# Optimization experiments

Hardware: AMD Instinct MI355X
Metric: run time of the kernel (lower is better)

The kernel has to match this reference:

```python
import jax, jax.numpy as jnp
import numpy as np

N = 1024
HID, STEM_CH = 256, 64
BN_OUT, ST_OUT, MLP = 128, 64, 256
MORPH, BN_WS, ST_WS = 31, 11, 31
FH = FW = 256
VH = VW = 1024
VIS_PS, FUSED_PS = 0.1, 0.4
DELTA_SCALE, EPS = 1.5, 1e-8


def _gauss(ws):
    y = np.linspace(-1.0, 1.0, ws)
    yy, xx = np.meshgrid(y, y, indexing='ij')
    g = np.exp(-(xx ** 2 + yy ** 2) / (2 * 0.4 ** 2))
    return jnp.asarray((g / g.sum())[None, None], dtype=jnp.float32)

BN_GAUSS = _gauss(BN_WS)
ST_GAUSS = _gauss(ST_WS)


def _gelu(x):
    return jax.nn.gelu(x, approximate=False)


def _softplus_inverse(x, eps=1e-6):
    x = jnp.maximum(x, eps)
    return x + jnp.log(-jnp.expm1(-x))


def _normalise(t, eps=EPS):
    t = jnp.maximum(t, 0.0)
    return t / (t.sum(axis=(-2, -1), keepdims=True) + eps)


def _extract_windows(fmap, pos, ws):
    # fmap: [1,C,H,W]; pos: [N,2] = (x,y) float pixel coords -> [N,C,ws,ws] via bilinear gather
    f = fmap[0]
    C, H, W = f.shape
    half = ws // 2
    offs = jnp.arange(ws, dtype=pos.dtype) - half
    xs = jnp.clip(pos[:, 0:1] + offs, 0.0, W - 1.0)  # [N,ws]
    ys = jnp.clip(pos[:, 1:2] + offs, 0.0, H - 1.0)
    x0 = jnp.clip(jnp.floor(xs), 0, W - 2).astype(jnp.int32)
    y0 = jnp.clip(jnp.floor(ys), 0, H - 2).astype(jnp.int32)
    wx = (xs - x0)[:, None, :]   # [N,1,ws]
    wy = (ys - y0)[:, :, None]   # [N,ws,1]
    X0, Y0 = x0[:, None, :], y0[:, :, None]
    v00 = f[:, Y0, X0]
    v01 = f[:, Y0, X0 + 1]
    v10 = f[:, Y0 + 1, X0]
    v11 = f[:, Y0 + 1, X0 + 1]   # each [C,N,ws,ws]
    out = (v00 * (1 - wy) * (1 - wx) + v01 * (1 - wy) * wx
           + v10 * wy * (1 - wx) + v11 * wy * wx)
    return out.transpose(1, 0, 2, 3)


def _convnext_block(x, dw_w, dw_b, ln_g, ln_b, pw1_w, pw1_b, pw2_w, pw2_b, gamma):
    C = x.shape[1]
    h = jax.lax.conv_general_dilated(x, dw_w, (1, 1), [(3, 3), (3, 3)],
        dimension_numbers=('NCHW', 'OIHW', 'NCHW'), feature_group_count=C)
    h = h + dw_b[None, :, None, None]
    h = h.transpose(0, 2, 3, 1)  # NHWC
    mu = h.mean(-1, keepdims=True)
    var = ((h - mu) ** 2).mean(-1, keepdims=True)
    h = (h - mu) / jnp.sqrt(var + 1e-6) * ln_g + ln_b
    h = _gelu(h @ pw1_w.T + pw1_b)
    h = (h @ pw2_w.T + pw2_b) * gamma
    return x + h.transpose(0, 3, 1, 2)


def _conv3x3(x, w, b):
    return jax.lax.conv_general_dilated(x, w, (1, 1), [(1, 1), (1, 1)],
        dimension_numbers=('NCHW', 'OIHW', 'NCHW')) + b[None, :, None, None]


def setup_inputs() -> dict:
    key = jax.random.key(0)
    ks = jax.random.split(key, 24)

    def w(i, shape, fan_in):
        return jax.random.normal(ks[i], shape, jnp.float32) / np.sqrt(fan_in)

    inp = {}
    inp['bottleneck'] = jax.random.normal(ks[0], (1, HID, FH, FW), jnp.float32)
    inp['vis_stem_features'] = jax.random.normal(ks[1], (1, STEM_CH, VH, VW), jnp.float32)
    inp['source_positions_vis'] = 20.0 + jax.random.uniform(ks[2], (N, 2), jnp.float32) * 980.0
    inp['init_morphology'] = jax.random.uniform(ks[3], (N, MORPH, MORPH), jnp.float32) + 1e-3
    # ConvNeXt block params
    inp['dw_w'] = w(4, (HID, 1, 7, 7), 49)
    inp['dw_b'] = jnp.zeros((HID,), jnp.float32)
    inp['ln_g'] = jnp.ones((HID,), jnp.float32)
    inp['ln_b'] = jnp.zeros((HID,), jnp.float32)
    inp['pw1_w'] = w(5, (4 * HID, HID), HID)
    inp['pw1_b'] = jnp.zeros((4 * HID,), jnp.float32)
    inp['pw2_w'] = w(6, (HID, 4 * HID), 4 * HID)
    inp['pw2_b'] = jnp.zeros((HID,), jnp.float32)
    inp['ls_gamma'] = 0.1 * jnp.ones((HID,), jnp.float32)
    # bottleneck 1x1 projection
    inp['bn_w'] = w(7, (BN_OUT, HID, 1, 1), HID)
    inp['bn_b'] = jnp.zeros((BN_OUT,), jnp.float32)
    # stem conv stack
    inp['st1_w'] = w(8, (ST_OUT, STEM_CH, 3, 3), 9 * STEM_CH)
    inp['st1_b'] = jnp.zeros((ST_OUT,), jnp.float32)
    inp['st2_w'] = w(9, (ST_OUT, ST_OUT, 3, 3), 9 * ST_OUT)
    inp['st2_b'] = jnp.zeros((ST_OUT,), jnp.float32)
    # trunk MLP
    feat_dim = BN_OUT + ST_OUT
    inp['tr1_w'] = w(10, (MLP, feat_dim), feat_dim)
    inp['tr1_b'] = jnp.zeros((MLP,), jnp.float32)
    inp['tr2_w'] = w(11, (MLP, MLP), MLP)
    inp['tr2_b'] = jnp.zeros((MLP,), jnp.float32)
    # morph delta head (small instead of exact zeros so the path is exercised)
    inp['md_w'] = 0.01 * w(12, (MORPH * MORPH, MLP), MLP)
    inp['md_b'] = jnp.zeros((MORPH * MORPH,), jnp.float32)
    inp['fused_h'] = FH
    inp['fused_w'] = FW
    inp['vis_h'] = VH
    inp['vis_w'] = VW
    return inp


def reference(bottleneck, vis_stem_features, source_positions_vis, init_morphology,
              dw_w, dw_b, ln_g, ln_b, pw1_w, pw1_b, pw2_w, pw2_b, ls_gamma,
              bn_w, bn_b, st1_w, st1_b, st2_w, st2_b,
              tr1_w, tr1_b, tr2_w, tr2_b, md_w, md_b,
              fused_h, fused_w, vis_h, vis_w):
    init_morph = _normalise(init_morphology)
    # VIS px -> bottleneck px (pixel-center-aligned affine between resolutions)
    s = VIS_PS / FUSED_PS
    pos_bn = (source_positions_vis + 0.5) * s - 0.5
    # bottleneck branch
    bn_win = _extract_windows(bottleneck, pos_bn, BN_WS)  # [N,HID,11,11]
    h = _convnext_block(bn_win, dw_w, dw_b, ln_g, ln_b, pw1_w, pw1_b, pw2_w, pw2_b, ls_gamma)
    h = _gelu(jnp.einsum('nchw,oc->nohw', h, bn_w[:, :, 0, 0]) + bn_b[None, :, None, None])
    bn_vec = (h * BN_GAUSS).sum(axis=(-2, -1))  # [N,BN_OUT]
    # stem branch
    st_win = _extract_windows(vis_stem_features, source_positions_vis, ST_WS)  # [N,64,31,31]
    g = _gelu(_conv3x3(st_win, st1_w, st1_b))
    g = _gelu(_conv3x3(g, st2_w, st2_b))
    st_vec = (g * ST_GAUSS).sum(axis=(-2, -1))  # [N,ST_OUT]
    feat = jnp.concatenate([bn_vec, st_vec], axis=1)
    hid = _gelu(feat @ tr1_w.T + tr1_b)
    hid = _gelu(hid @ tr2_w.T + tr2_b)
    delta = jnp.tanh(hid @ md_w.T + md_b).reshape(init_morph.shape)
    base_logits = _softplus_inverse(jnp.maximum(init_morph, EPS), eps=EPS)
    morphology = _normalise(jax.nn.softplus(base_logits + DELTA_SCALE * delta))
    return morphology, delta, feat
```

## Files before the change

### kernel.cpp

```cpp
#include <hip/hip_runtime.h>
#include <math.h>

#define N_SRC 1024
#define VHW 1024
#define FHW 256
#define MQ 30976

typedef __attribute__((ext_vector_type(8))) short short8;
typedef __attribute__((ext_vector_type(4))) float f32x4;

#define MFMA_B16(a,b,c) __builtin_amdgcn_mfma_f32_16x16x32_bf16((a),(b),(c),0,0,0)

__device__ __forceinline__ float gelu_f(float x){
  return 0.5f * x * (1.0f + erff(x * 0.70710678118654752440f));
}
__device__ __forceinline__ unsigned short f2bf(float f){
  union { float f; unsigned u; } x; x.f = f;
  unsigned r = x.u + 0x7fffu + ((x.u >> 16) & 1u);
  return (unsigned short)(r >> 16);
}
__device__ __forceinline__ float bf2f(unsigned short h){
  union { unsigned u; float f; } x; x.u = ((unsigned)h) << 16;
  return x.f;
}

__global__ void k_gauss(float* __restrict__ gbn, float* __restrict__ gst){
  __shared__ double red[256];
  int t = threadIdx.x;
  {
    double v = 0.0;
    if (t < 121){
      int r = t / 11, c = t % 11;
      double y = -1.0 + 2.0 * (double)r / 10.0;
      double x = -1.0 + 2.0 * (double)c / 10.0;
      v = exp(-(x*x + y*y) / (2.0 * 0.4 * 0.4));
    }
    red[t] = v; __syncthreads();
    for (int s = 128; s > 0; s >>= 1){ if (t < s) red[t] += red[t+s]; __syncthreads(); }
    double sum = red[0];
    __syncthreads();
    if (t < 121) gbn[t] = (float)(v / sum);
    __syncthreads();
  }
  {
    double vals[4]; double loc = 0.0;
    #pragma unroll
    for (int i = 0; i < 4; ++i){
      int j = t + 256*i;
      double v = 0.0;
      if (j < 961){
        int r = j / 31, c = j % 31;
        double y = -1.0 + 2.0 * (double)r / 30.0;
        double x = -1.0 + 2.0 * (double)c / 30.0;
        v = exp(-(x*x + y*y) / (2.0 * 0.4 * 0.4));
      }
      vals[i] = v; loc += v;
    }
    red[t] = loc; __syncthreads();
    for (int s = 128; s > 0; s >>= 1){ if (t < s) red[t] += red[t+s]; __syncthreads(); }
    double sum = red[0];
    __syncthreads();
    #pragma unroll
    for (int i = 0; i < 4; ++i){
      int j = t + 256*i;
      if (j < 961) gst[j] = (float)(vals[i] / sum);
    }
  }
}

__global__ void k_trans(const float* __restrict__ pw1_w, const float* __restrict__ pw2_w,
                        const float* __restrict__ bn_w,
                        const float* __restrict__ st1_w, const float* __restrict__ st2_w,
                        unsigned short* __restrict__ W1b, unsigned short* __restrict__ W2b,
                        unsigned short* __restrict__ bnWb,
                        unsigned short* __restrict__ Wc1, unsigned short* __restrict__ Wc2){
  int stride = gridDim.x * blockDim.x;
  int i0 = blockIdx.x * blockDim.x + threadIdx.x;
  for (int e = i0; e < 256*1024; e += stride) W1b[e] = f2bf(pw1_w[e]);
  for (int e = i0; e < 256*1024; e += stride) W2b[e] = f2bf(pw2_w[e]);
  for (int e = i0; e < 128*256; e += stride) bnWb[e] = f2bf(bn_w[e]);
  for (int e = i0; e < 64*576; e += stride){
    int co = e / 576, r = e % 576, d = r >> 6, ci = r & 63;
    Wc1[e] = f2bf(st1_w[(co*64 + ci)*9 + d]);
    Wc2[e] = f2bf(st2_w[(co*64 + ci)*9 + d]);
  }
}


__global__ __launch_bounds__(256) void k_stg(
    const float* __restrict__ vis, const float* __restrict__ pos,
    unsigned short* __restrict__ v_win)
{
  int b = blockIdx.x;
  int n = b >> 1, h = b & 1;
  float px = pos[2*n], py = pos[2*n + 1];
  int e0 = h * 3844;
  for (int e = e0 + threadIdx.x; e < e0 + 3844; e += 256){
    int cg = e / 961, p = e - cg*961;
    int r = p / 31, c = p - r*31;
    float xsf = fminf(fmaxf(px + (float)(c - 15), 0.f), 1023.f);
    float ysf = fminf(fmaxf(py + (float)(r - 15), 0.f), 1023.f);
    int x0 = min((int)xsf, 1022);
    int y0 = min((int)ysf, 1022);
    float wx = xsf - (float)x0, wy = ysf - (float)y0;
    float w00 = (1.f-wy)*(1.f-wx), w01 = (1.f-wy)*wx;
    float w10 = wy*(1.f-wx),       w11 = wy*wx;
    size_t off = (size_t)y0*VHW + x0;
    const float* bp = vis + (size_t)(cg*8)*(VHW*VHW) + off;
    short8 v;
    #pragma unroll
    for (int i = 0; i < 8; ++i){
      const float* bb = bp + (size_t)i*(VHW*VHW);
      v[i] = (short)f2bf(bb[0]*w00 + bb[1]*w01 + bb[VHW]*w10 + bb[VHW+1]*w11);
    }
    *(short8*)&v_win[((size_t)cg*(1024*961) + (size_t)n*961 + p)*8] = v;
  }
}

__device__ __forceinline__ void conv_tiles_mfma(
    const unsigned short* __restrict__ in_t, const short8* B0, const short8* B1,
    int pb0, int pb1, int lk, f32x4& a00, f32x4& a01, f32x4& a10, f32x4& a11)
{
  #pragma unroll
  for (int ks = 0; ks < 18; ++ks){
    const int d = ks >> 1;
    const int dy = d / 3, dx = d - dy*3;
    const int cofs = (ks & 1)*32;
    int ci0 = cofs + lk*8;
    int p0 = pb0 + dy*33 + dx, p1 = pb1 + dy*33 + dx;
    short8 A0 = *(const short8*)&in_t[(p0*64 + ci0) ^ ((p0 & 7) << 3)];
    short8 A1 = *(const short8*)&in_t[(p1*64 + ci0) ^ ((p1 & 7) << 3)];
    a00 = MFMA_B16(A0, B0[ks], a00);
    a01 = MFMA_B16(A0, B1[ks], a01);
    a10 = MFMA_B16(A1, B0[ks], a10);
    a11 = MFMA_B16(A1, B1[ks], a11);
  }
}

__global__ __launch_bounds__(512, 4) void k_stc1(
    const unsigned short* __restrict__ v_win,
    const unsigned short* __restrict__ Wc1, const float* __restrict__ st1_b,
    unsigned short* __restrict__ g1)
{
  __shared__ unsigned short in_t[594*64];
  int n = blockIdx.x, band = blockIdx.y;
  int t = threadIdx.x;
  int w = t >> 6, l = t & 63, lr = l & 15, lk = l >> 4;
  int ybase = band*16 - 1;
  int rows_out = band ? 15 : 16;

  for (int c = t; c < 594*8; c += 512){
    int p = c >> 3, cg = c & 7;
    int gr = p / 33, gc = p - gr*33;
    int yy = ybase + gr, xx = gc - 1;
    short8 v = {0,0,0,0,0,0,0,0};
    if (yy >= 0 && yy < 31 && xx >= 0 && xx < 31)
      v = *(const short8*)&v_win[((size_t)cg*(1024*961) + (size_t)n*961 + yy*31 + xx)*8];
    *(short8*)&in_t[(p*64 + cg*8) ^ ((p & 7) << 3)] = v;
  }
  __syncthreads();

  int co0 = (w & 1) * 32;
  short8 B0[18], B1[18];
  #pragma unroll
  for (int ks = 0; ks < 18; ++ks){
    B0[ks] = *(const short8*)&Wc1[(co0 + lr)*576 + ks*32 + lk*8];
    B1[ks] = *(const short8*)&Wc1[(co0 + 16 + lr)*576 + ks*32 + lk*8];
  }
  int npos = rows_out * 31;
  int ntiles = (npos + 15) >> 4;
  int mstart = (w >> 1) * 8;
  int mend = min(mstart + 8, ntiles);
  float bc0 = st1_b[co0 + lr], bc1 = st1_b[co0 + 16 + lr];

  for (int mt = mstart; mt < mend; mt += 2){
    int s0 = min(mt*16 + lr, npos - 1);
    int s1 = min(mt*16 + 16 + lr, npos - 1);
    int ly0 = s0 / 31, x0p = s0 - ly0*31;
    int ly1 = s1 / 31, x1p = s1 - ly1*31;
    int pb0 = ly0*33 + x0p, pb1 = ly1*33 + x1p;
    f32x4 a00 = {0,0,0,0}, a01 = {0,0,0,0}, a10 = {0,0,0,0}, a11 = {0,0,0,0};
    conv_tiles_mfma(in_t, B0, B1, pb0, pb1, lk, a00, a01, a10, a11);
    #pragma unroll
    for (int i = 0; i < 4; ++i){
      int spo = mt*16 + lk*4 + i;
      if (spo < npos){
        int ly = spo / 31, xx = spo - ly*31;
        size_t o = ((size_t)(n*961 + (band*16 + ly)*31 + xx)) * 64;
        g1[o + co0 + lr]      = f2bf(gelu_f(a00[i] + bc0));
        g1[o + co0 + 16 + lr] = f2bf(gelu_f(a01[i] + bc1));
      }
      int sp1 = spo + 16;
      if (sp1 < npos && mt + 1 < ntiles){
        int ly = sp1 / 31, xx = sp1 - ly*31;
        size_t o = ((size_t)(n*961 + (band*16 + ly)*31 + xx)) * 64;
        g1[o + co0 + lr]      = f2bf(gelu_f(a10[i] + bc0));
        g1[o + co0 + 16 + lr] = f2bf(gelu_f(a11[i] + bc1));
      }
    }
  }
}

__global__ __launch_bounds__(512, 4) void k_stc2(
    const unsigned short* __restrict__ g1, const float* __restrict__ gst,
    const unsigned short* __restrict__ Wc2, const float* __restrict__ st2_b,
    float* __restrict__ st_vec)
{
  __shared__ unsigned short in_t[594*64];
  int n = blockIdx.x, band = blockIdx.y;
  int t = threadIdx.x;
  int w = t >> 6, l = t & 63, lr = l & 15, lk = l >> 4;
  int ybase = band*16 - 1;
  int rows_out = band ? 15 : 16;

  for (int c = t; c < 594*8; c += 512){
    int p = c >> 3, ci0 = (c & 7) * 8;
    int gr = p / 33, gc = p - gr*33;
    int yy = ybase + gr, xx = gc - 1;
    short8 v = {0,0,0,0,0,0,0,0};
    if (yy >= 0 && yy < 31 && xx >= 0 && xx < 31)
      v = *(const short8*)&g1[((size_t)(n*961 + yy*31 + xx))*64 + ci0];
    *(short8*)&in_t[(p*64 + ci0) ^ ((p & 7) << 3)] = v;
  }
  __syncthreads();

  int co0 = (w & 1) * 32;
  short8 B0[18], B1[18];
  #pragma unroll
  for (int ks = 0; ks < 18; ++ks){
    B0[ks] = *(const short8*)&Wc2[(co0 + lr)*576 + ks*32 + lk*8];
    B1[ks] = *(const short8*)&Wc2[(co0 + 16 + lr)*576 + ks*32 + lk*8];
  }
  int npos = rows_out * 31;
  int ntiles = (npos + 15) >> 4;
  int mstart = (w >> 1) * 8;
  int mend = min(mstart + 8, ntiles);
  float bc0 = st2_b[co0 + lr], bc1 = st2_b[co0 + 16 + lr];
  float vacc0 = 0.f, vacc1 = 0.f;

  for (int mt = mstart; mt < mend; mt += 2){
    int s0 = min(mt*16 + lr, npos - 1);
    int s1 = min(mt*16 + 16 + lr, npos - 1);
    int ly0 = s0 / 31, x0p = s0 - ly0*31;
    int ly1 = s1 / 31, x1p = s1 - ly1*31;
    int pb0 = ly0*33 + x0p, pb1 = ly1*33 + x1p;
    f32x4 a00 = {0,0,0,0}, a01 = {0,0,0,0}, a10 = {0,0,0,0}, a11 = {0,0,0,0};
    conv_tiles_mfma(in_t, B0, B1, pb0, pb1, lk, a00, a01, a10, a11);
    #pragma unroll
    for (int i = 0; i < 4; ++i){
      int spo = mt*16 + lk*4 + i;
      if (spo < npos){
        int ly = spo / 31, xx = spo - ly*31;
        float wt = gst[(band*16 + ly)*31 + xx];
        vacc0 += wt * gelu_f(a00[i] + bc0);
        vacc1 += wt * gelu_f(a01[i] + bc1);
      }
      int sp1 = spo + 16;
      if (sp1 < npos && mt + 1 < ntiles){
        int ly = sp1 / 31, xx = sp1 - ly*31;
        float wt = gst[(band*16 + ly)*31 + xx];
        vacc0 += wt * gelu_f(a10[i] + bc0);
        vacc1 += wt * gelu_f(a11[i] + bc1);
      }
    }
  }
  vacc0 += __shfl_xor(vacc0, 16); vacc0 += __shfl_xor(vacc0, 32);
  vacc1 += __shfl_xor(vacc1, 16); vacc1 += __shfl_xor(vacc1, 32);
  if (lk == 0){
    atomicAdd(&st_vec[n*64 + co0 + lr], vacc0);
    atomicAdd(&st_vec[n*64 + co0 + 16 + lr], vacc1);
  }
}

__global__ __launch_bounds__(512, 4) void k_bnpre(
  const float* __restrict__ bott, const float* __restrict__ pos,
  const float* __restrict__ dw_w, const float* __restrict__ dw_b,
  unsigned short* __restrict__ x_bf, unsigned short* __restrict__ dcob)
{
  __shared__ float xt[128*123];
  __shared__ float wt4[121*4];
  __shared__ int   wo[121];
  int n = blockIdx.x, ch0 = blockIdx.y * 128;
  int t = threadIdx.x;
  float pbx = (pos[2*n]   + 0.5f)*0.25f - 0.5f;
  float pby = (pos[2*n+1] + 0.5f)*0.25f - 0.5f;

  if (t < 121){
    int r = t / 11, c = t - r*11;
    float xsf = fminf(fmaxf(pbx + (float)(c-5), 0.f), 255.f);
    float ysf = fminf(fmaxf(pby + (float)(r-5), 0.f), 255.f);
    int x0 = min((int)xsf, 254);
    int y0 = min((int)ysf, 254);
    float wx = xsf - (float)x0, wy = ysf - (float)y0;
    wo[t] = y0*FHW + x0;
    wt4[t*4+0] = (1.f-wy)*(1.f-wx);
    wt4[t*4+1] = (1.f-wy)*wx;
    wt4[t*4+2] = wy*(1.f-wx);
    wt4[t*4+3] = wy*wx;
  }
  __syncthreads();

  for (int e = t; e < 128*121; e += 512){
    int ch = e / 121, p = e - ch*121;
    const float* b = bott + (size_t)(ch0 + ch)*(FHW*FHW) + wo[p];
    float4 w = *(const float4*)&wt4[p*4];
    xt[ch*123 + p] = b[0]*w.x + b[1]*w.y + b[FHW]*w.z + b[FHW+1]*w.w;
  }
  __syncthreads();

  for (int e = t; e < 121*64; e += 512){
    int row = e >> 6, cp = (e & 63) << 1;
    float v0 = xt[cp*123 + row], v1 = xt[(cp+1)*123 + row];
    unsigned pk = (unsigned)f2bf(v0) | ((unsigned)f2bf(v1) << 16);
    *(unsigned*)&x_bf[(((size_t)n*121 + row) << 8) + ch0 + cp] = pk;
  }

  int ch = t & 127, part = t >> 7;
  float w[49];
  #pragma unroll
  for (int k = 0; k < 49; ++k) w[k] = dw_w[(ch0 + ch)*49 + k];
  float bias = dw_b[ch0 + ch];
  const float* xc = &xt[ch*123];
  for (int sp = part; sp < 121; sp += 4){
    int r = sp / 11, c = sp - r*11;
    float a = bias;
    #pragma unroll
    for (int dy = 0; dy < 7; ++dy){
      int ry = r + dy - 3;
      bool okr = (ry >= 0) && (ry < 11);
      #pragma unroll
      for (int dx = 0; dx < 7; ++dx){
        int cx = c + dx - 3;
        float xv = (okr && cx >= 0 && cx < 11) ? xc[ry*11 + cx] : 0.f;
        a = fmaf(xv, w[dy*7 + dx], a);
      }
    }
    dcob[(((size_t)n*121 + sp) << 8) + ch0 + ch] = f2bf(a);
  }
}

__global__ __launch_bounds__(256) void k_ln(
  const unsigned short* __restrict__ dcob, const float* __restrict__ ln_g, const float* __restrict__ ln_b,
  unsigned short* __restrict__ normb)
{
  int m = blockIdx.x*4 + (threadIdx.x >> 6);
  int lane = threadIdx.x & 63;
  ushort4 raw = *(const ushort4*)&dcob[(size_t)m*256 + lane*4];
  float4 v = { bf2f(raw.x), bf2f(raw.y), bf2f(raw.z), bf2f(raw.w) };
  float s  = v.x+v.y+v.z+v.w;
  float ss = v.x*v.x + v.y*v.y + v.z*v.z + v.w*v.w;
  #pragma unroll
  for (int off = 32; off; off >>= 1){ s += __shfl_xor(s, off); ss += __shfl_xor(ss, off); }
  float mu  = s * 0.00390625f;
  float var = ss * 0.00390625f - mu*mu;
  float rstd = 1.0f / sqrtf(var + 1e-6f);
  float4 g = *(const float4*)&ln_g[lane*4];
  float4 b = *(const float4*)&ln_b[lane*4];
  ushort4 o;
  o.x = f2bf((v.x-mu)*rstd*g.x + b.x);
  o.y = f2bf((v.y-mu)*rstd*g.y + b.y);
  o.z = f2bf((v.z-mu)*rstd*g.z + b.z);
  o.w = f2bf((v.w-mu)*rstd*g.w + b.w);
  *(ushort4*)&normb[(size_t)m*256 + lane*4] = o;
}


__global__ __launch_bounds__(256, 3) void k_gemm1(
  const unsigned short* __restrict__ A, const unsigned short* __restrict__ B,
  const float* __restrict__ b1, unsigned short* __restrict__ H)
{
  __shared__ __align__(16) unsigned short sm[16384];
  unsigned short* As = sm;
  unsigned short* Bs = sm + 8192;
  int t = threadIdx.x, lane = t & 63, w = t >> 6;
  int lr = lane & 15, lk = lane >> 4;
  int p = blockIdx.x;
  int L = (p & 7) * 242 + (p >> 3);
  int m0 = (L >> 3) * 128, n0 = (L & 7) * 128;

  f32x4 acc[2][8];
  #pragma unroll
  for (int i = 0; i < 2; ++i)
    #pragma unroll
    for (int j = 0; j < 8; ++j) acc[i][j] = (f32x4){0,0,0,0};

  for (int ks = 0; ks < 4; ++ks){
    if (ks) __syncthreads();
    #pragma unroll
    for (int it = 0; it < 4; ++it){
      int j = t + it*256;
      int r = j >> 3, c = j & 7;
      int k8 = c ^ (r & 7);
      *(short8*)&As[j*8] = *(const short8*)&A[(size_t)(m0 + r)*256 + ks*64 + k8*8];
      *(short8*)&Bs[j*8] = *(const short8*)&B[(size_t)(n0 + r)*256 + ks*64 + k8*8];
    }
    __syncthreads();
    #pragma unroll
    for (int kk = 0; kk < 2; ++kk){
      int k8a = kk*4 + lk;
      short8 af[2];
      #pragma unroll
      for (int i = 0; i < 2; ++i){
        int ra = w*32 + i*16 + lr;
        af[i] = *(const short8*)&As[(ra*8 + (k8a ^ (ra & 7)))*8];
      }
      #pragma unroll
      for (int j = 0; j < 8; ++j){
        int rb = j*16 + lr;
        short8 bf = *(const short8*)&Bs[(rb*8 + (k8a ^ (rb & 7)))*8];
        acc[0][j] = MFMA_B16(af[0], bf, acc[0][j]);
        acc[1][j] = MFMA_B16(af[1], bf, acc[1][j]);
      }
    }
  }
  __syncthreads();
  #pragma unroll
  for (int i = 0; i < 2; ++i)
    #pragma unroll
    for (int j = 0; j < 8; ++j){
      int col = j*16 + lr;
      float bb = b1[n0 + col];
      #pragma unroll
      for (int q = 0; q < 4; ++q){
        int row = w*32 + i*16 + lk*4 + q;
        sm[row*128 + col] = f2bf(gelu_f(acc[i][j][q] + bb));
      }
    }
  __syncthreads();
  #pragma unroll
  for (int it = 0; it < 8; ++it){
    int e = t + it*256;
    int row = e >> 4, c8 = e & 15;
    *(short8*)&H[(size_t)(m0 + row)*1024 + n0 + c8*8] = *(const short8*)&sm[row*128 + c8*8];
  }
}

__global__ __launch_bounds__(256, 4) void k_gemm2(
  const unsigned short* __restrict__ A, const unsigned short* __restrict__ B,
  const float* __restrict__ b2v, const float* __restrict__ lsg,
  const unsigned short* __restrict__ xres, unsigned short* __restrict__ Y)
{
  __shared__ __align__(16) unsigned short sm[16384];
  unsigned short* As = sm;
  unsigned short* Bs = sm + 8192;
  int t = threadIdx.x, lane = t & 63, w = t >> 6;
  int lr = lane & 15, lk = lane >> 4;
  int p = blockIdx.x;
  int L = (p & 7) * 121 + (p >> 3);
  int m0 = (L >> 2) * 128, n0 = (L & 3) * 64;

  f32x4 acc[2][4];
  #pragma unroll
  for (int i = 0; i < 2; ++i)
    #pragma unroll
    for (int j = 0; j < 4; ++j) acc[i][j] = (f32x4){0,0,0,0};

  for (int ks = 0; ks < 16; ++ks){
    if (ks) __syncthreads();
    #pragma unroll
    for (int it = 0; it < 4; ++it){
      int j = t + it*256;
      int r = j >> 3, c = j & 7;
      int k8 = c ^ (r & 7);
      *(short8*)&As[j*8] = *(const short8*)&A[(size_t)(m0 + r)*1024 + ks*64 + k8*8];
    }
    #pragma unroll
    for (int it = 0; it < 2; ++it){
      int j = t + it*256;
      int r = j >> 3, c = j & 7;
      int k8 = c ^ (r & 7);
      *(short8*)&Bs[j*8] = *(const short8*)&B[(size_t)(n0 + r)*1024 + ks*64 + k8*8];
    }
    __syncthreads();
    #pragma unroll
    for (int kk = 0; kk < 2; ++kk){
      int k8a = kk*4 + lk;
      short8 af[2];
      #pragma unroll
      for (int i = 0; i < 2; ++i){
        int ra = w*32 + i*16 + lr;
        af[i] = *(const short8*)&As[(ra*8 + (k8a ^ (ra & 7)))*8];
      }
      #pragma unroll
      for (int j = 0; j < 4; ++j){
        int rb = j*16 + lr;
        short8 bf = *(const short8*)&Bs[(rb*8 + (k8a ^ (rb & 7)))*8];
        acc[0][j] = MFMA_B16(af[0], bf, acc[0][j]);
        acc[1][j] = MFMA_B16(af[1], bf, acc[1][j]);
      }
    }
  }
  __syncthreads();
  float* Cs = (float*)sm;
  #pragma unroll
  for (int i = 0; i < 2; ++i)
    #pragma unroll
    for (int j = 0; j < 4; ++j){
      int col = j*16 + lr;
      #pragma unroll
      for (int q = 0; q < 4; ++q){
        int row = w*32 + i*16 + lk*4 + q;
        Cs[row*64 + col] = acc[i][j][q];
      }
    }
  __syncthreads();
  #pragma unroll
  for (int it = 0; it < 8; ++it){
    int e4 = t + it*256;
    int row = e4 >> 4, c4 = (e4 & 15) * 4;
    float4 cv = *(const float4*)&Cs[row*64 + c4];
    size_t grow = (size_t)(m0 + row);
    ushort4 xr = *(const ushort4*)&xres[grow*256 + n0 + c4];
    float4 bb = *(const float4*)&b2v[n0 + c4];
    float4 gm = *(const float4*)&lsg[n0 + c4];
    ushort4 o;
    o.x = f2bf(fmaf(cv.x + bb.x, gm.x, bf2f(xr.x)));
    o.y = f2bf(fmaf(cv.y + bb.y, gm.y, bf2f(xr.y)));
    o.z = f2bf(fmaf(cv.z + bb.z, gm.z, bf2f(xr.z)));
    o.w = f2bf(fmaf(cv.w + bb.w, gm.w, bf2f(xr.w)));
    *(ushort4*)&Y[grow*256 + n0 + c4] = o;
  }
}

__global__ __launch_bounds__(256) void k_bnvec(
  const unsigned short* __restrict__ yb, const unsigned short* __restrict__ bnWb,
  const float* __restrict__ bn_b, const float* __restrict__ gbn, float* __restrict__ bn_vec)
{
  int n = blockIdx.x, t = threadIdx.x;
  int w = t >> 6, l = t & 63, lr = l & 15, lk = l >> 4;
  f32x4 acc[8][2];
  #pragma unroll
  for (int mt = 0; mt < 8; ++mt){ acc[mt][0] = (f32x4){0,0,0,0}; acc[mt][1] = (f32x4){0,0,0,0}; }

  #pragma unroll
  for (int ks = 0; ks < 8; ++ks){
    short8 b0 = *(const short8*)&bnWb[(size_t)(w*32 + lr)*256 + ks*32 + lk*8];
    short8 b1 = *(const short8*)&bnWb[(size_t)(w*32 + 16 + lr)*256 + ks*32 + lk*8];
    #pragma unroll
    for (int mt = 0; mt < 8; ++mt){
      int row = min(mt*16 + lr, 120);
      short8 a = *(const short8*)&yb[((size_t)n*121 + row)*256 + ks*32 + lk*8];
      acc[mt][0] = MFMA_B16(a, b0, acc[mt][0]);
      acc[mt][1] = MFMA_B16(a, b1, acc[mt][1]);
    }
  }

  float s0 = 0.f, s1 = 0.f;
  float bb0 = bn_b[w*32 + lr], bb1 = bn_b[w*32 + 16 + lr];
  #pragma unroll
  for (int mt = 0; mt < 8; ++mt)
    #pragma unroll
    for (int i = 0; i < 4; ++i){
      int row = mt*16 + lk*4 + i;
      if (row < 121){
        float g = gbn[row];
        s0 += g * gelu_f(acc[mt][0][i] + bb0);
        s1 += g * gelu_f(acc[mt][1][i] + bb1);
      }
    }
  s0 += __shfl_xor(s0, 16); s0 += __shfl_xor(s0, 32);
  s1 += __shfl_xor(s1, 16); s1 += __shfl_xor(s1, 32);
  if (lk == 0){
    bn_vec[n*128 + w*32 + lr] = s0;
    bn_vec[n*128 + w*32 + 16 + lr] = s1;
  }
}

__global__ __launch_bounds__(256) void k_head(
  const float* __restrict__ bn_vec, const float* __restrict__ st_vec,
  const float* __restrict__ tr1_w, const float* __restrict__ tr1_b,
  const float* __restrict__ tr2_w, const float* __restrict__ tr2_b,
  const float* __restrict__ md_w, const float* __restrict__ md_b,
  const float* __restrict__ init_m,
  float* __restrict__ out)
{
  __shared__ float feat4[4*192];
  __shared__ float h14[4*256];
  __shared__ float h24[4*256];
  __shared__ float dlt4[4*961];
  __shared__ float yv4[4*961];
  int t = threadIdx.x;
  int n0 = blockIdx.x * 4;
  float* morph_out = out;
  float* delta_out = out + 984064;
  float* feat_out  = out + 1968128;

  for (int e = t; e < 4*192; e += 256){
    int ni = e / 192, j = e - ni*192;
    float v = (j < 128) ? bn_vec[(n0+ni)*128 + j] : st_vec[(n0+ni)*64 + j - 128];
    feat4[e] = v;
    feat_out[(size_t)(n0+ni)*192 + j] = v;
  }
  __syncthreads();
  {
    float a0 = tr1_b[t], a1 = a0, a2 = a0, a3 = a0;
    const float* wr = &tr1_w[t*192];
    for (int k = 0; k < 192; ++k){
      float wk = wr[k];
      a0 = fmaf(feat4[k],       wk, a0);
      a1 = fmaf(feat4[192 + k], wk, a1);
      a2 = fmaf(feat4[384 + k], wk, a2);
      a3 = fmaf(feat4[576 + k], wk, a3);
    }
    h14[t] = gelu_f(a0); h14[256 + t] = gelu_f(a1);
    h14[512 + t] = gelu_f(a2); h14[768 + t] = gelu_f(a3);
  }
  __syncthreads();
  {
    float a0 = tr2_b[t], a1 = a0, a2 = a0, a3 = a0;
    const float* wr = &tr2_w[t*256];
    for (int k = 0; k < 256; ++k){
      float wk = wr[k];
      a0 = fmaf(h14[k],       wk, a0);
      a1 = fmaf(h14[256 + k], wk, a1);
      a2 = fmaf(h14[512 + k], wk, a2);
      a3 = fmaf(h14[768 + k], wk, a3);
    }
    h24[t] = gelu_f(a0); h24[256 + t] = gelu_f(a1);
    h24[512 + t] = gelu_f(a2); h24[768 + t] = gelu_f(a3);
  }
  __syncthreads();
  for (int j = t; j < 961; j += 256){
    float b = md_b[j];
    float a0 = b, a1 = b, a2 = b, a3 = b;
    const float* wr = &md_w[(size_t)j*256];
    for (int k = 0; k < 256; ++k){
      float wk = wr[k];
      a0 = fmaf(h24[k],       wk, a0);
      a1 = fmaf(h24[256 + k], wk, a1);
      a2 = fmaf(h24[512 + k], wk, a2);
      a3 = fmaf(h24[768 + k], wk, a3);
    }
    float d0 = tanhf(a0), d1 = tanhf(a1), d2 = tanhf(a2), d3 = tanhf(a3);
    dlt4[j] = d0; dlt4[961 + j] = d1; dlt4[1922 + j] = d2; dlt4[2883 + j] = d3;
    delta_out[(size_t)(n0+0)*961 + j] = d0;
    delta_out[(size_t)(n0+1)*961 + j] = d1;
    delta_out[(size_t)(n0+2)*961 + j] = d2;
    delta_out[(size_t)(n0+3)*961 + j] = d3;
  }
  __syncthreads();

  int g = t >> 6, l64 = t & 63;
  int n = n0 + g;
  const float* im = &init_m[(size_t)n*961];
  float loc = 0.f;
  for (int j = l64; j < 961; j += 64) loc += fmaxf(im[j], 0.f);
  #pragma unroll
  for (int off = 32; off; off >>= 1) loc += __shfl_xor(loc, off);
  float s0 = loc + 1e-8f;
  float loc2 = 0.f;
  for (int j = l64; j < 961; j += 64){
    float imn = fmaxf(im[j], 0.f) / s0;
    float x = fmaxf(imn, 1e-8f);
    float base = x + logf(-expm1f(-x));
    float z = base + 1.5f * dlt4[g*961 + j];
    float y = fmaxf(z, 0.f) + log1pf(expf(-fabsf(z)));
    yv4[g*961 + j] = y;
    loc2 += y;
  }
  #pragma unroll
  for (int off = 32; off; off >>= 1) loc2 += __shfl_xor(loc2, off);
  float s1 = loc2 + 1e-8f;
  for (int j = l64; j < 961; j += 64)
    morph_out[(size_t)n*961 + j] = yv4[g*961 + j] / s1;
}

extern "C" void kernel_launch(void* const* d_in, const int* in_sizes, int n_in,
                              void* d_out, int out_size, void* d_ws, size_t ws_size,
                              hipStream_t stream)
{
  const float* bott = (const float*)d_in[0];
  const float* vis  = (const float*)d_in[1];
  const float* pos  = (const float*)d_in[2];
  const float* initm= (const float*)d_in[3];
  const float* dw_w = (const float*)d_in[4];
  const float* dw_b = (const float*)d_in[5];
  const float* ln_g = (const float*)d_in[6];
  const float* ln_b = (const float*)d_in[7];
  const float* pw1_w= (const float*)d_in[8];
  const float* pw1_b= (const float*)d_in[9];
  const float* pw2_w= (const float*)d_in[10];
  const float* pw2_b= (const float*)d_in[11];
  const float* lsg  = (const float*)d_in[12];
  const float* bn_w = (const float*)d_in[13];
  const float* bn_b = (const float*)d_in[14];
  const float* st1_w= (const float*)d_in[15];
  const float* st1_b= (const float*)d_in[16];
  const float* st2_w= (const float*)d_in[17];
  const float* st2_b= (const float*)d_in[18];
  const float* tr1_w= (const float*)d_in[19];
  const float* tr1_b= (const float*)d_in[20];
  const float* tr2_w= (const float*)d_in[21];
  const float* tr2_b= (const float*)d_in[22];
  const float* md_w = (const float*)d_in[23];
  const float* md_b = (const float*)d_in[24];

  char* ws = (char*)d_ws;
  unsigned short* v_win = (unsigned short*)(ws);
  unsigned short* dcob  = (unsigned short*)(ws);
  unsigned short* Hq    = (unsigned short*)(ws);
  unsigned short* yb    = (unsigned short*)(ws + 63438848);
  unsigned short* g1    = (unsigned short*)(ws + 126877696);
  unsigned short* x_bf  = (unsigned short*)(ws + 126877696);
  unsigned short* normb = (unsigned short*)(ws + 190316544);
  char* S = ws + 253755392;
  float* st_vec = (float*)(S);
  float* bn_vec = (float*)(S + 262144);
  float* gbn    = (float*)(S + 786432);
  float* gst    = (float*)(S + 786944);
  unsigned short* W1b  = (unsigned short*)(S + 791040);
  unsigned short* W2b  = (unsigned short*)(S + 1315328);
  unsigned short* Wc1  = (unsigned short*)(S + 1839616);
  unsigned short* Wc2  = (unsigned short*)(S + 1913344);
  unsigned short* bnWb = (unsigned short*)(S + 1987072);

  hipMemsetAsync(st_vec, 0, 1024*64*sizeof(float), stream);
  k_gauss<<<1, 256, 0, stream>>>(gbn, gst);
  k_trans<<<256, 256, 0, stream>>>(pw1_w, pw2_w, bn_w, st1_w, st2_w, W1b, W2b, bnWb, Wc1, Wc2);

  k_stg<<<2048, 256, 0, stream>>>(vis, pos, v_win);
  k_stc1<<<dim3(1024, 2), 512, 0, stream>>>(v_win, Wc1, st1_b, g1);
  k_stc2<<<dim3(1024, 2), 512, 0, stream>>>(g1, gst, Wc2, st2_b, st_vec);

  k_bnpre<<<dim3(1024, 2), 512, 0, stream>>>(bott, pos, dw_w, dw_b, x_bf, dcob);
  k_ln<<<30976, 256, 0, stream>>>(dcob, ln_g, ln_b, normb);

  for (int q = 0; q < 4; ++q){
    size_t ro = (size_t)q * MQ;
    k_gemm1<<<1936, 256, 0, stream>>>(normb + ro*256, W1b, pw1_b, Hq);
    k_gemm2<<<968, 256, 0, stream>>>(Hq, W2b, pw2_b, lsg, x_bf + ro*256, yb + ro*256);
  }
  k_bnvec<<<1024, 256, 0, stream>>>(yb, bnWb, bn_b, gbn, bn_vec);

  k_head<<<256, 256, 0, stream>>>(bn_vec, st_vec, tr1_w, tr1_b, tr2_w, tr2_b,
                                  md_w, md_b, initm, (float*)d_out);
}
```

Before: 1.415 ms.

## Fuse the two stem 3x3 convolutions into one kernel via an LDS intermediate

Merges k_stc1 and k_stc2 into a single kernel. Each band block computes conv1 over an 18-row halo region (recomputing the overlapping rows between bands) and writes the GELU output as bf16 into shared memory, which conv2 then reads directly. This removes the g1 global round trip and one kernel launch. In exchange it does some redundant conv1 work, LDS use roughly doubles and launch bounds drop to 1 block per SM, which lowers occupancy.

After: 1.267 ms. 10.5% less time.

```diff
diff --git a/kernel.cpp b/kernel.cpp
--- a/kernel.cpp
+++ b/kernel.cpp
@@ -137,138 +137,133 @@
   }
 }
 
-__global__ __launch_bounds__(512, 4) void k_stc1(
+__global__ __launch_bounds__(512, 1) void k_stconv(
     const unsigned short* __restrict__ v_win,
     const unsigned short* __restrict__ Wc1, const float* __restrict__ st1_b,
-    unsigned short* __restrict__ g1)
-{
-  __shared__ unsigned short in_t[594*64];
+    const unsigned short* __restrict__ Wc2, const float* __restrict__ st2_b,
+    const float* __restrict__ gst, float* __restrict__ st_vec)
+{
+  __shared__ __align__(16) unsigned short As[660*64];
+  __shared__ __align__(16) unsigned short Bs[594*64];
   int n = blockIdx.x, band = blockIdx.y;
   int t = threadIdx.x;
   int w = t >> 6, l = t & 63, lr = l & 15, lk = l >> 4;
-  int ybase = band*16 - 1;
+  int ybaseV = band*16 - 2;
+  int ybaseG = band*16 - 1;
   int rows_out = band ? 15 : 16;
 
-  for (int c = t; c < 594*8; c += 512){
+  for (int c = t; c < 660*8; c += 512){
     int p = c >> 3, cg = c & 7;
     int gr = p / 33, gc = p - gr*33;
-    int yy = ybase + gr, xx = gc - 1;
+    int yy = ybaseV + gr, xx = gc - 1;
     short8 v = {0,0,0,0,0,0,0,0};
     if (yy >= 0 && yy < 31 && xx >= 0 && xx < 31)
       v = *(const short8*)&v_win[((size_t)cg*(1024*961) + (size_t)n*961 + yy*31 + xx)*8];
-    *(short8*)&in_t[(p*64 + cg*8) ^ ((p & 7) << 3)] = v;
+    *(short8*)&As[(p*64 + cg*8) ^ ((p & 7) << 3)] = v;
+  }
+  {
+    short8 z = {0,0,0,0,0,0,0,0};
+    for (int c = t; c < 594*8; c += 512)
+      *(short8*)&Bs[c*8] = z;
   }
   __syncthreads();
 
   int co0 = (w & 1) * 32;
-  short8 B0[18], B1[18];
-  #pragma unroll
-  for (int ks = 0; ks < 18; ++ks){
-    B0[ks] = *(const short8*)&Wc1[(co0 + lr)*576 + ks*32 + lk*8];
-    B1[ks] = *(const short8*)&Wc1[(co0 + 16 + lr)*576 + ks*32 + lk*8];
-  }
-  int npos = rows_out * 31;
-  int ntiles = (npos + 15) >> 4;
-  int mstart = (w >> 1) * 8;
-  int mend = min(mstart + 8, ntiles);
-  float bc0 = st1_b[co0 + lr], bc1 = st1_b[co0 + 16 + lr];
-
-  for (int mt = mstart; mt < mend; mt += 2){
-    int s0 = min(mt*16 + lr, npos - 1);
-    int s1 = min(mt*16 + 16 + lr, npos - 1);
-    int ly0 = s0 / 31, x0p = s0 - ly0*31;
-    int ly1 = s1 / 31, x1p = s1 - ly1*31;
-    int pb0 = ly0*33 + x0p, pb1 = ly1*33 + x1p;
-    f32x4 a00 = {0,0,0,0}, a01 = {0,0,0,0}, a10 = {0,0,0,0}, a11 = {0,0,0,0};
-    conv_tiles_mfma(in_t, B0, B1, pb0, pb1, lk, a00, a01, a10, a11);
-    #pragma unroll
-    for (int i = 0; i < 4; ++i){
-      int spo = mt*16 + lk*4 + i;
-      if (spo < npos){
-        int ly = spo / 31, xx = spo - ly*31;
-        size_t o = ((size_t)(n*961 + (band*16 + ly)*31 + xx)) * 64;
-        g1[o + co0 + lr]      = f2bf(gelu_f(a00[i] + bc0));
-        g1[o + co0 + 16 + lr] = f2bf(gelu_f(a01[i] + bc1));
-      }
-      int sp1 = spo + 16;
-      if (sp1 < npos && mt + 1 < ntiles){
-        int ly = sp1 / 31, xx = sp1 - ly*31;
-        size_t o = ((size_t)(n*961 + (band*16 + ly)*31 + xx)) * 64;
-        g1[o + co0 + lr]      = f2bf(gelu_f(a10[i] + bc0));
-        g1[o + co0 + 16 + lr] = f2bf(gelu_f(a11[i] + bc1));
-      }
-    }
-  }
-}
-
-__global__ __launch_bounds__(512, 4) void k_stc2(
-    const unsigned short* __restrict__ g1, const float* __restrict__ gst,
-    const unsigned short* __restrict__ Wc2, const float* __restrict__ st2_b,
-    float* __restrict__ st_vec)
-{
-  __shared__ unsigned short in_t[594*64];
-  int n = blockIdx.x, band = blockIdx.y;
-  int t = threadIdx.x;
-  int w = t >> 6, l = t & 63, lr = l & 15, lk = l >> 4;
-  int ybase = band*16 - 1;
-  int rows_out = band ? 15 : 16;
-
-  for (int c = t; c < 594*8; c += 512){
-    int p = c >> 3, ci0 = (c & 7) * 8;
-    int gr = p / 33, gc = p - gr*33;
-    int yy = ybase + gr, xx = gc - 1;
-    short8 v = {0,0,0,0,0,0,0,0};
-    if (yy >= 0 && yy < 31 && xx >= 0 && xx < 31)
-      v = *(const short8*)&g1[((size_t)(n*961 + yy*31 + xx))*64 + ci0];
-    *(short8*)&in_t[(p*64 + ci0) ^ ((p & 7) << 3)] = v;
-  }
-  __syncthreads();
-
-  int co0 = (w & 1) * 32;
-  short8 B0[18], B1[18];
-  #pragma unroll
-  for (int ks = 0; ks < 18; ++ks){
-    B0[ks] = *(const short8*)&Wc2[(co0 + lr)*576 + ks*32 + lk*8];
-    B1[ks] = *(const short8*)&Wc2[(co0 + 16 + lr)*576 + ks*32 + lk*8];
-  }
-  int npos = rows_out * 31;
-  int ntiles = (npos + 15) >> 4;
-  int mstart = (w >> 1) * 8;
-  int mend = min(mstart + 8, ntiles);
-  float bc0 = st2_b[co0 + lr], bc1 = st2_b[co0 + 16 + lr];
-  float vacc0 = 0.f, vacc1 = 0.f;
-
-  for (int mt = mstart; mt < mend; mt += 2){
-    int s0 = min(mt*16 + lr, npos - 1);
-    int s1 = min(mt*16 + 16 + lr, npos - 1);
-    int ly0 = s0 / 31, x0p = s0 - ly0*31;
-    int ly1 = s1 / 31, x1p = s1 - ly1*31;
-    int pb0 = ly0*33 + x0p, pb1 = ly1*33 + x1p;
-    f32x4 a00 = {0,0,0,0}, a01 = {0,0,0,0}, a10 = {0,0,0,0}, a11 = {0,0,0,0};
-    conv_tiles_mfma(in_t, B0, B1, pb0, pb1, lk, a00, a01, a10, a11);
-    #pragma unroll
-    for (int i = 0; i < 4; ++i){
-      int spo = mt*16 + lk*4 + i;
-      if (spo < npos){
-        int ly = spo / 31, xx = spo - ly*31;
-        float wt = gst[(band*16 + ly)*31 + xx];
-        vacc0 += wt * gelu_f(a00[i] + bc0);
-        vacc1 += wt * gelu_f(a01[i] + bc1);
-      }
-      int sp1 = spo + 16;
-      if (sp1 < npos && mt + 1 < ntiles){
-        int ly = sp1 / 31, xx = sp1 - ly*31;
-        float wt = gst[(band*16 + ly)*31 + xx];
-        vacc0 += wt * gelu_f(a10[i] + bc0);
-        vacc1 += wt * gelu_f(a11[i] + bc1);
-      }
-    }
-  }
-  vacc0 += __shfl_xor(vacc0, 16); vacc0 += __shfl_xor(vacc0, 32);
-  vacc1 += __shfl_xor(vacc1, 16); vacc1 += __shfl_xor(vacc1, 32);
-  if (lk == 0){
-    atomicAdd(&st_vec[n*64 + co0 + lr], vacc0);
-    atomicAdd(&st_vec[n*64 + co0 + 16 + lr], vacc1);
+
+  {
+    short8 B0[18], B1[18];
+    #pragma unroll
+    for (int ks = 0; ks < 18; ++ks){
+      B0[ks] = *(const short8*)&Wc1[(co0 + lr)*576 + ks*32 + lk*8];
+      B1[ks] = *(const short8*)&Wc1[(co0 + 16 + lr)*576 + ks*32 + lk*8];
+    }
+    const int npos1 = 18*31;
+    const int ntiles1 = 35;
+    int mstart = (w >> 1) * 10;
+    int mend = min(mstart + 10, ntiles1);
+    float bc0 = st1_b[co0 + lr], bc1 = st1_b[co0 + 16 + lr];
+
+    for (int mt = mstart; mt < mend; mt += 2){
+      int s0 = min(mt*16 + lr, npos1 - 1);
+      int s1 = min(mt*16 + 16 + lr, npos1 - 1);
+      int ly0 = s0 / 31, x0p = s0 - ly0*31;
+      int ly1 = s1 / 31, x1p = s1 - ly1*31;
+      int pb0 = ly0*33 + x0p, pb1 = ly1*33 + x1p;
+      f32x4 a00 = {0,0,0,0}, a01 = {0,0,0,0}, a10 = {0,0,0,0}, a11 = {0,0,0,0};
+      conv_tiles_mfma(As, B0, B1, pb0, pb1, lk, a00, a01, a10, a11);
+      #pragma unroll
+      for (int i = 0; i < 4; ++i){
+        int spo = mt*16 + lk*4 + i;
+        if (spo < npos1){
+          int ly = spo / 31, xx = spo - ly*31;
+          int yy1 = ybaseG + ly;
+          if (yy1 >= 0 && yy1 <= 30){
+            int pB = ly*33 + xx + 1;
+            Bs[(pB*64 + co0 + lr) ^ ((pB & 7) << 3)]      = f2bf(gelu_f(a00[i] + bc0));
+            Bs[(pB*64 + co0 + 16 + lr) ^ ((pB & 7) << 3)] = f2bf(gelu_f(a01[i] + bc1));
+          }
+        }
+        int sp1 = spo + 16;
+        if (sp1 < npos1 && mt + 1 < ntiles1){
+          int ly = sp1 / 31, xx = sp1 - ly*31;
+          int yy1 = ybaseG + ly;
+          if (yy1 >= 0 && yy1 <= 30){
+            int pB = ly*33 + xx + 1;
+            Bs[(pB*64 + co0 + lr) ^ ((pB & 7) << 3)]      = f2bf(gelu_f(a10[i] + bc0));
+            Bs[(pB*64 + co0 + 16 + lr) ^ ((pB & 7) << 3)] = f2bf(gelu_f(a11[i] + bc1));
+          }
+        }
+      }
+    }
+  }
+  __syncthreads();
+
+  {
+    short8 B0[18], B1[18];
+    #pragma unroll
+    for (int ks = 0; ks < 18; ++ks){
+      B0[ks] = *(const short8*)&Wc2[(co0 + lr)*576 + ks*32 + lk*8];
+      B1[ks] = *(const short8*)&Wc2[(co0 + 16 + lr)*576 + ks*32 + lk*8];
+    }
+    int npos = rows_out * 31;
+    int ntiles = (npos + 15) >> 4;
+    int mstart = (w >> 1) * 8;
+    int mend = min(mstart + 8, ntiles);
+    float bc0 = st2_b[co0 + lr], bc1 = st2_b[co0 + 16 + lr];
+    float vacc0 = 0.f, vacc1 = 0.f;
+
+    for (int mt = mstart; mt < mend; mt += 2){
+      int s0 = min(mt*16 + lr, npos - 1);
+      int s1 = min(mt*16 + 16 + lr, npos - 1);
+      int ly0 = s0 / 31, x0p = s0 - ly0*31;
+      int ly1 = s1 / 31, x1p = s1 - ly1*31;
+      int pb0 = ly0*33 + x0p, pb1 = ly1*33 + x1p;
+      f32x4 a00 = {0,0,0,0}, a01 = {0,0,0,0}, a10 = {0,0,0,0}, a11 = {0,0,0,0};
+      conv_tiles_mfma(Bs, B0, B1, pb0, pb1, lk, a00, a01, a10, a11);
+      #pragma unroll
+      for (int i = 0; i < 4; ++i){
+        int spo = mt*16 + lk*4 + i;
+        if (spo < npos){
+          int ly = spo / 31, xx = spo - ly*31;
+          float wt = gst[(band*16 + ly)*31 + xx];
+          vacc0 += wt * gelu_f(a00[i] + bc0);
+          vacc1 += wt * gelu_f(a01[i] + bc1);
+        }
+        int sp1 = spo + 16;
+        if (sp1 < npos && mt + 1 < ntiles){
+          int ly = sp1 / 31, xx = sp1 - ly*31;
+          float wt = gst[(band*16 + ly)*31 + xx];
+          vacc0 += wt * gelu_f(a10[i] + bc0);
+          vacc1 += wt * gelu_f(a11[i] + bc1);
+        }
+      }
+    }
+    vacc0 += __shfl_xor(vacc0, 16); vacc0 += __shfl_xor(vacc0, 32);
+    vacc1 += __shfl_xor(vacc1, 16); vacc1 += __shfl_xor(vacc1, 32);
+    if (lk == 0){
+      atomicAdd(&st_vec[n*64 + co0 + lr], vacc0);
+      atomicAdd(&st_vec[n*64 + co0 + 16 + lr], vacc1);
+    }
   }
 }
 
@@ -700,7 +695,6 @@
   unsigned short* dcob  = (unsigned short*)(ws);
   unsigned short* Hq    = (unsigned short*)(ws);
   unsigned short* yb    = (unsigned short*)(ws + 63438848);
-  unsigned short* g1    = (unsigned short*)(ws + 126877696);
   unsigned short* x_bf  = (unsigned short*)(ws + 126877696);
   unsigned short* normb = (unsigned short*)(ws + 190316544);
   char* S = ws + 253755392;
@@ -719,8 +713,7 @@
   k_trans<<<256, 256, 0, stream>>>(pw1_w, pw2_w, bn_w, st1_w, st2_w, W1b, W2b, bnWb, Wc1, Wc2);
 
   k_stg<<<2048, 256, 0, stream>>>(vis, pos, v_win);
-  k_stc1<<<dim3(1024, 2), 512, 0, stream>>>(v_win, Wc1, st1_b, g1);
-  k_stc2<<<dim3(1024, 2), 512, 0, stream>>>(g1, gst, Wc2, st2_b, st_vec);
+  k_stconv<<<dim3(1024, 2), 512, 0, stream>>>(v_win, Wc1, st1_b, Wc2, st2_b, gst, st_vec);
 
   k_bnpre<<<dim3(1024, 2), 512, 0, stream>>>(bott, pos, dw_w, dw_b, x_bf, dcob);
   k_ln<<<30976, 256, 0, stream>>>(dcob, ln_g, ln_b, normb);
```
